# Kernel tuning notes

Measured on AMD Instinct MI355X. Metric: run time of the kernel, lower is better.

## Reference

```python
import jax, jax.numpy as jnp
import numpy as np

N = 50000      # nodes
E = 800000     # edges (avg degree 16)
IN = 100       # in_channels (hard-coded LayerNorm(100))
H = 128        # hidden_channels
G = 512        # num graphs in batch
C = 2          # num_classes
EPS = 1e-5     # LayerNorm eps (torch default)


def setup_inputs() -> dict:
    key = jax.random.key(0)
    ks = jax.random.split(key, 12)
    x = jax.random.normal(ks[0], (N, IN), dtype=jnp.float32)
    edge_index = jax.random.randint(ks[1], (2, E), 0, N, dtype=jnp.int64)
    edge_weight = jax.random.uniform(ks[2], (E,), dtype=jnp.float32)
    batch = jnp.sort(jax.random.randint(ks[3], (N,), 0, G, dtype=jnp.int64))
    # LayerNorm params (identity init, as torch)
    ln_g0, ln_b0 = jnp.ones((IN,), jnp.float32), jnp.zeros((IN,), jnp.float32)
    ln_g1, ln_b1 = jnp.ones((H,), jnp.float32), jnp.zeros((H,), jnp.float32)
    ln_g2, ln_b2 = jnp.ones((H,), jnp.float32), jnp.zeros((H,), jnp.float32)
    # GCNConv weights (glorot-ish scale) and biases
    W0 = jax.random.normal(ks[4], (IN, H), jnp.float32) / np.float32(np.sqrt(IN))
    b0 = jnp.zeros((H,), jnp.float32)
    W1 = jax.random.normal(ks[5], (H, H), jnp.float32) / np.float32(np.sqrt(H))
    b1 = jnp.zeros((H,), jnp.float32)
    W2 = jax.random.normal(ks[6], (H, H), jnp.float32) / np.float32(np.sqrt(H))
    b2 = jnp.zeros((H,), jnp.float32)
    # Final classifier
    Wlin = jax.random.normal(ks[7], (H, C), jnp.float32) / np.float32(np.sqrt(H))
    blin = jnp.zeros((C,), jnp.float32)
    return {"x": x, "edge_index": edge_index, "edge_weight": edge_weight,
            "batch": batch,
            "ln_g0": ln_g0, "ln_b0": ln_b0, "ln_g1": ln_g1, "ln_b1": ln_b1,
            "ln_g2": ln_g2, "ln_b2": ln_b2,
            "W0": W0, "b0": b0, "W1": W1, "b1": b1, "W2": W2, "b2": b2,
            "Wlin": Wlin, "blin": blin}


def _layernorm(h, g, b):
    m = jnp.mean(h, axis=-1, keepdims=True)
    v = jnp.mean(jnp.square(h - m), axis=-1, keepdims=True)
    return (h - m) * jax.lax.rsqrt(v + EPS) * g + b


def _gcn_conv(h, W, b, src, dst, edge_weight):
    # GCNConv(normalize=False): linear transform, edge gather scaled by
    # edge_weight, scatter-add to destination nodes, plus bias.
    hW = h @ W                                  # [N, H]
    msg = hW[src] * edge_weight[:, None]        # [E, H]
    agg = jax.ops.segment_sum(msg, dst, num_segments=N)  # [N, H]
    return agg + b


def reference(x, edge_index, edge_weight, batch,
              ln_g0, ln_b0, ln_g1, ln_b1, ln_g2, ln_b2,
              W0, b0, W1, b1, W2, b2, Wlin, blin):
    src, dst = edge_index[0], edge_index[1]
    layers = [(ln_g0, ln_b0, W0, b0), (ln_g1, ln_b1, W1, b1), (ln_g2, ln_b2, W2, b2)]
    h = x
    for (g, bb, W, cb) in layers:
        h = _layernorm(h, g, bb)
        h = _gcn_conv(h, W, cb, src, dst, edge_weight)
        h = jax.nn.relu(h)  # dropout is identity in eval mode
    # global mean pool over graphs
    sums = jax.ops.segment_sum(h, batch, num_segments=G)                       # [G, H]
    cnt = jax.ops.segment_sum(jnp.ones((N, 1), h.dtype), batch, num_segments=G)
    pooled = sums / jnp.maximum(cnt, 1.0)
    return pooled @ Wlin + blin  # [G, C]
```

## Files before the change

kernel.cpp:

```cpp
#include <hip/hip_runtime.h>
#include <hip/hip_bf16.h>

#define NN 50000
#define NE 800000
#define NG 512
#define HD 128
#define EPS 1e-5f
#define L1B 196
#define EPB 4096
#define NL1 ((NE + EPB - 1) / EPB)

typedef __attribute__((ext_vector_type(8))) short short8;
typedef __attribute__((ext_vector_type(4))) float f32x4;

__device__ __forceinline__ float bfu(unsigned short u) {
    return __uint_as_float((unsigned)u << 16);
}

__global__ __launch_bounds__(256) void k_init(int* __restrict__ gtot,
                                              float* __restrict__ pooled,
                                              const float* __restrict__ W0,
                                              const float* __restrict__ W1,
                                              const float* __restrict__ W2,
                                              __hip_bfloat16* __restrict__ bp) {
    const int i = blockIdx.x * 256 + threadIdx.x;
    if (i < L1B) gtot[i] = 0;
    if (i < NG * HD) pooled[i] = 0.f;
    if (i < 3 * 2048) {
        const int layer = i >> 11;
        const int f     = i & 2047;
        const int tile  = f >> 8, kk = (f >> 6) & 3, lane = f & 63;
        const int col   = tile * 16 + (lane & 15);
        const int kbase = kk * 32 + ((lane >> 4) << 3);
        const float* W  = (layer == 0) ? W0 : (layer == 1) ? W1 : W2;
        const int Klim  = (layer == 0) ? 100 : 128;
        alignas(16) __hip_bfloat16 o[8];
#pragma unroll
        for (int j = 0; j < 8; ++j) {
            const int k = kbase + j;
            o[j] = __float2bfloat16((k < Klim) ? W[(size_t)k * HD + col] : 0.f);
        }
        *(float4*)&bp[(size_t)i * 8] = *(const float4*)o;
    }
}

__global__ __launch_bounds__(256) void k_histL1(const int* __restrict__ dstv,
                                                int* __restrict__ gtot, int E) {
    __shared__ int h[L1B];
    const int t  = threadIdx.x;
    const int e0 = blockIdx.x * EPB;
    const int e1 = (e0 + EPB < E) ? (e0 + EPB) : E;
    for (int i = t; i < L1B; i += 256) h[i] = 0;
    __syncthreads();
    for (int e = e0 + t; e < e1; e += 256) atomicAdd(&h[dstv[e] >> 8], 1);
    __syncthreads();
    for (int i = t; i < L1B; i += 256)
        if (h[i]) atomicAdd(&gtot[i], h[i]);
}

__global__ __launch_bounds__(256) void k_scan196(const int* __restrict__ gtot,
                                                 int* __restrict__ gbase,
                                                 int* __restrict__ gcursor,
                                                 int* __restrict__ row_ptr) {
    __shared__ int s[256];
    const int t = threadIdx.x;
    const int v = (t < L1B) ? gtot[t] : 0;
    s[t] = v;
    __syncthreads();
    for (int off = 1; off < 256; off <<= 1) {
        int u = (t >= off) ? s[t - off] : 0;
        __syncthreads();
        s[t] += u;
        __syncthreads();
    }
    const int ex = s[t] - v;
    if (t < L1B) { gbase[t] = ex; gcursor[t] = ex; }
    if (t == 0) { gbase[L1B] = NE; row_ptr[NN] = NE; }
}

__global__ __launch_bounds__(256) void k_binL1(const int* __restrict__ srcv,
                                               const int* __restrict__ dstv,
                                               const float* __restrict__ ewt,
                                               int* __restrict__ gcursor,
                                               int2* __restrict__ stage, int E) {
    __shared__ int hist[L1B], lstart[L1B], gbase[L1B], lcur[L1B];
    __shared__ int s[256];
    __shared__ int2 lsort[EPB];
    const int t  = threadIdx.x;
    const int e0 = blockIdx.x * EPB;
    const int e1 = (e0 + EPB < E) ? (e0 + EPB) : E;
    for (int i = t; i < L1B; i += 256) hist[i] = 0;
    __syncthreads();
    for (int e = e0 + t; e < e1; e += 256)
        atomicAdd(&hist[dstv[e] >> 8], 1);
    __syncthreads();
    {
        const int v = (t < L1B) ? hist[t] : 0;
        s[t] = v;
        __syncthreads();
        for (int off = 1; off < 256; off <<= 1) {
            int u = (t >= off) ? s[t - off] : 0;
            __syncthreads();
            s[t] += u;
            __syncthreads();
        }
        if (t < L1B) {
            const int ex = s[t] - v;
            lstart[t] = ex;
            lcur[t]   = ex;
            gbase[t]  = v ? atomicAdd(&gcursor[t], v) : 0;
        }
    }
    __syncthreads();
    for (int e = e0 + t; e < e1; e += 256) {
        const int d = dstv[e];
        const int r = atomicAdd(&lcur[d >> 8], 1);
        lsort[r] = make_int2((d << 16) | srcv[e], __float_as_int(ewt[e]));
    }
    __syncthreads();
    const int n = e1 - e0;
    for (int i = t; i < n; i += 256) {
        const int2 el = lsort[i];
        const unsigned b = ((unsigned)el.x) >> 24;
        stage[gbase[b] + (i - lstart[b])] = el;
    }
}

__global__ __launch_bounds__(256) void k_binL2(const int2* __restrict__ stage,
                                               const int* __restrict__ gbase,
                                               int* __restrict__ row_ptr,
                                               int2* __restrict__ cw) {
    __shared__ int cnt[256], s[256], cur[256];
    const int t    = threadIdx.x;
    const int b    = blockIdx.x;
    const int d0   = b << 8;
    const int nd   = (NN - d0 < 256) ? (NN - d0) : 256;
    const int base = gbase[b];
    const int end  = gbase[b + 1];
    cnt[t] = 0;
    __syncthreads();
    for (int i = base + t; i < end; i += 256) {
        const unsigned dst = ((unsigned)stage[i].x) >> 16;
        atomicAdd(&cnt[dst - d0], 1);
    }
    __syncthreads();
    {
        const int v = cnt[t];
        s[t] = v;
        __syncthreads();
        for (int off = 1; off < 256; off <<= 1) {
            int u = (t >= off) ? s[t - off] : 0;
            __syncthreads();
            s[t] += u;
            __syncthreads();
        }
        const int ex = base + s[t] - v;
        cur[t] = ex;
        if (t < nd) row_ptr[d0 + t] = ex;
    }
    __syncthreads();
    for (int i = base + t; i < end; i += 256) {
        const int2 el = stage[i];
        const unsigned dst = ((unsigned)el.x) >> 16;
        const int p = atomicAdd(&cur[dst - d0], 1);
        cw[p] = make_int2(el.x & 0xFFFF, el.y);
    }
}

__device__ __forceinline__ void mfma_gemm_store(const __hip_bfloat16 (*hb)[136],
                                                const __hip_bfloat16* __restrict__ bp,
                                                __hip_bfloat16* __restrict__ hwb,
                                                int t, int r0) {
    const int wave = t >> 6, lane = t & 63;
    const int rw   = wave * 16;
    const int arow = rw + (lane & 15);
    const int acol = ((lane >> 4) << 3);
    short8 a[4];
#pragma unroll
    for (int kk = 0; kk < 4; ++kk)
        a[kk] = *(const short8*)&hb[arow][kk * 32 + acol];

    f32x4 acc[8] = {};
    const short8* bfr = (const short8*)bp;
#pragma unroll
    for (int tile = 0; tile < 8; ++tile) {
#pragma unroll
        for (int kk = 0; kk < 4; ++kk) {
            const short8 bb = bfr[(tile * 4 + kk) * 64 + lane];
            acc[tile] = __builtin_amdgcn_mfma_f32_16x16x32_bf16(a[kk], bb, acc[tile], 0, 0, 0);
        }
    }
    const int baser = r0 + rw + ((lane >> 4) << 2);
    const int bcol  = lane & 15;
#pragma unroll
    for (int tile = 0; tile < 8; ++tile) {
        const int col = tile * 16 + bcol;
#pragma unroll
        for (int j = 0; j < 4; ++j) {
            const int row = baser + j;
            if (row < NN) hwb[(size_t)row * HD + col] = __float2bfloat16(acc[tile][j]);
        }
    }
}

__global__ __launch_bounds__(256, 3) void k_ln_gemm_f32(const float* __restrict__ hin,
                                                        const float* __restrict__ g,
                                                        const float* __restrict__ b,
                                                        const __hip_bfloat16* __restrict__ bp,
                                                        __hip_bfloat16* __restrict__ hwb) {
    constexpr int K  = 100;
    constexpr int SK = K + 4;
    __shared__ float hs[64][SK];
    __shared__ __hip_bfloat16 hb[64][136];
    const int t  = threadIdx.x;
    const int r0 = blockIdx.x * 64;
    {
        const float4* src4 = (const float4*)(hin + (size_t)r0 * K);
        const int valid_rows = (NN - r0 < 64) ? (NN - r0) : 64;
        const int maxf = valid_rows * K;
        for (int i = t; i < 64 * K / 4; i += 256) {
            int f = i * 4;
            float4 v = (f < maxf) ? src4[i] : make_float4(0.f, 0.f, 0.f, 0.f);
            int r = f / K, k = f - r * K;
            *(float4*)&hs[r][k] = v;
        }
    }
    __syncthreads();
    {
        const int row = t >> 2, l = t & 3;
        float s = 0.f, s2 = 0.f;
        for (int k = l; k < K; k += 4) { float v = hs[row][k]; s += v; s2 += v * v; }
        s  += __shfl_xor(s, 1);  s2 += __shfl_xor(s2, 1);
        s  += __shfl_xor(s, 2);  s2 += __shfl_xor(s2, 2);
        const float mean = s / (float)K;
        const float var  = s2 / (float)K - mean * mean;
        const float rstd = rsqrtf(var + EPS);
        for (int k = l; k < K; k += 4)
            hb[row][k] = __float2bfloat16((hs[row][k] - mean) * rstd * g[k] + b[k]);
        for (int k = K + l; k < 128; k += 4)
            hb[row][k] = __float2bfloat16(0.f);
    }
    __syncthreads();
    mfma_gemm_store(hb, bp, hwb, t, r0);
}

__global__ __launch_bounds__(256, 4) void k_ln_gemm_b16(const __hip_bfloat16* __restrict__ hin,
                                                        const float* __restrict__ g,
                                                        const float* __restrict__ b,
                                                        const __hip_bfloat16* __restrict__ bp,
                                                        __hip_bfloat16* __restrict__ hwb) {
    __shared__ __hip_bfloat16 hb[64][136];
    const int t  = threadIdx.x;
    const int r0 = blockIdx.x * 64;
    {
        const float4* src4 = (const float4*)(hin + (size_t)r0 * HD);
        const int valid_rows = (NN - r0 < 64) ? (NN - r0) : 64;
        const int maxv = valid_rows * 16;
        for (int i = t; i < 1024; i += 256) {
            float4 v = (i < maxv) ? src4[i] : make_float4(0.f, 0.f, 0.f, 0.f);
            const int r = i >> 4, k = (i & 15) * 8;
            *(float4*)&hb[r][k] = v;
        }
    }
    __syncthreads();
    {
        const int row = t >> 2, l = t & 3;
        float s = 0.f, s2 = 0.f;
        for (int k = l; k < 128; k += 4) {
            const float v = __bfloat162float(hb[row][k]);
            s += v; s2 += v * v;
        }
        s  += __shfl_xor(s, 1);  s2 += __shfl_xor(s2, 1);
        s  += __shfl_xor(s, 2);  s2 += __shfl_xor(s2, 2);
        const float mean = s / 128.f;
        const float var  = s2 / 128.f - mean * mean;
        const float rstd = rsqrtf(var + EPS);
        for (int k = l; k < 128; k += 4)
            hb[row][k] = __float2bfloat16((__bfloat162float(hb[row][k]) - mean) * rstd * g[k] + b[k]);
    }
    __syncthreads();
    mfma_gemm_store(hb, bp, hwb, t, r0);
}

__device__ __forceinline__ float4 agg_row(const __hip_bfloat16* __restrict__ hwb,
                                          const int2* __restrict__ cw,
                                          const float* __restrict__ bias,
                                          int e0, int e1, size_t coff) {
    float4 acc = {0.f, 0.f, 0.f, 0.f};
    int e = e0;
    for (; e + 8 <= e1; e += 8) {
        int2 c[8];
#pragma unroll
        for (int j = 0; j < 8; ++j) c[j] = cw[e + j];
        ushort4 r[8];
#pragma unroll
        for (int j = 0; j < 8; ++j)
            r[j] = *(const ushort4*)(hwb + (size_t)c[j].x * HD + coff);
#pragma unroll
        for (int j = 0; j < 8; ++j) {
            const float w = __int_as_float(c[j].y);
            acc.x += w * bfu(r[j].x);
            acc.y += w * bfu(r[j].y);
            acc.z += w * bfu(r[j].z);
            acc.w += w * bfu(r[j].w);
        }
    }
    if (e + 4 <= e1) {
        int2 c[4];
#pragma unroll
        for (int j = 0; j < 4; ++j) c[j] = cw[e + j];
        ushort4 r[4];
#pragma unroll
        for (int j = 0; j < 4; ++j)
            r[j] = *(const ushort4*)(hwb + (size_t)c[j].x * HD + coff);
#pragma unroll
        for (int j = 0; j < 4; ++j) {
            const float w = __int_as_float(c[j].y);
            acc.x += w * bfu(r[j].x);
            acc.y += w * bfu(r[j].y);
            acc.z += w * bfu(r[j].z);
            acc.w += w * bfu(r[j].w);
        }
        e += 4;
    }
    for (; e < e1; ++e) {
        const int2 c = cw[e];
        const float w = __int_as_float(c.y);
        const ushort4 rv = *(const ushort4*)(hwb + (size_t)c.x * HD + coff);
        acc.x += w * bfu(rv.x);
        acc.y += w * bfu(rv.y);
        acc.z += w * bfu(rv.z);
        acc.w += w * bfu(rv.w);
    }
    const float4 bb = *(const float4*)(bias + coff);
    float4 o;
    o.x = fmaxf(acc.x + bb.x, 0.f);
    o.y = fmaxf(acc.y + bb.y, 0.f);
    o.z = fmaxf(acc.z + bb.z, 0.f);
    o.w = fmaxf(acc.w + bb.w, 0.f);
    return o;
}

__global__ __launch_bounds__(256) void k_aggregate(const __hip_bfloat16* __restrict__ hwb,
                                                   const int* __restrict__ row_ptr,
                                                   const int2* __restrict__ cw,
                                                   const float* __restrict__ bias,
                                                   __hip_bfloat16* __restrict__ hout, int n) {
    const int t    = threadIdx.x;
    const int grp  = t >> 5;
    const int lane = t & 31;
    const int node = blockIdx.x * 8 + grp;
    if (node >= n) return;
    const size_t coff = (size_t)lane * 4;
    float4 o = agg_row(hwb, cw, bias, row_ptr[node], row_ptr[node + 1], coff);
    alignas(8) __hip_bfloat16 ob[4] = {
        __float2bfloat16(o.x), __float2bfloat16(o.y),
        __float2bfloat16(o.z), __float2bfloat16(o.w)};
    *(ushort4*)(hout + (size_t)node * HD + coff) = *(const ushort4*)ob;
}

__global__ __launch_bounds__(256) void k_aggpool(const __hip_bfloat16* __restrict__ hwb,
                                                 const int* __restrict__ row_ptr,
                                                 const int2* __restrict__ cw,
                                                 const float* __restrict__ bias,
                                                 const int* __restrict__ batch,
                                                 float* __restrict__ pooled, int n) {
    __shared__ float lds[8][128];
    __shared__ int gof[8];
    const int t    = threadIdx.x;
    const int grp  = t >> 5;
    const int lane = t & 31;
    const int node = blockIdx.x * 8 + grp;
    const size_t coff = (size_t)lane * 4;
    float4 o = {0.f, 0.f, 0.f, 0.f};
    if (node < n)
        o = agg_row(hwb, cw, bias, row_ptr[node], row_ptr[node + 1], coff);
    *(float4*)&lds[grp][lane * 4] = o;
    if (lane == 0) gof[grp] = (node < n) ? batch[node] : -1;
    __syncthreads();
    if (t < 128) {
        float sum = 0.f;
        int curg = gof[0];
#pragma unroll
        for (int r = 0; r < 8; ++r) {
            const int gr = gof[r];
            if (gr != curg) {
                if (curg >= 0) atomicAdd(&pooled[curg * HD + t], sum);
                sum = 0.f;
                curg = gr;
            }
            if (gr >= 0) sum += lds[r][t];
        }
        if (curg >= 0) atomicAdd(&pooled[curg * HD + t], sum);
    }
}

__global__ __launch_bounds__(128) void k_linout(const float* __restrict__ pooled,
                                                const int* __restrict__ batch,
                                                const float* __restrict__ Wlin,
                                                const float* __restrict__ blin,
                                                float* __restrict__ out, int n) {
    __shared__ float red[2][128];
    const int gph = blockIdx.x;
    const int c   = threadIdx.x;
    int lo = 0, hi = n;
    while (lo < hi) { int mid = (lo + hi) >> 1; if (batch[mid] < gph) lo = mid + 1; else hi = mid; }
    const int start = lo;
    hi = n;
    while (lo < hi) { int mid = (lo + hi) >> 1; if (batch[mid] < gph + 1) lo = mid + 1; else hi = mid; }
    const float cnt = (float)(lo - start);
    const float pv = pooled[gph * HD + c] / fmaxf(cnt, 1.0f);
    red[0][c] = pv * Wlin[c * 2 + 0];
    red[1][c] = pv * Wlin[c * 2 + 1];
    __syncthreads();
    for (int off = 64; off; off >>= 1) {
        if (c < off) { red[0][c] += red[0][c + off]; red[1][c] += red[1][c + off]; }
        __syncthreads();
    }
    if (c == 0) {
        out[gph * 2 + 0] = red[0][0] + blin[0];
        out[gph * 2 + 1] = red[1][0] + blin[1];
    }
}

extern "C" void kernel_launch(void* const* d_in, const int* in_sizes, int n_in,
                              void* d_out, int out_size, void* d_ws, size_t ws_size,
                              hipStream_t stream) {
    const float* x     = (const float*)d_in[0];
    const int*   ei    = (const int*)d_in[1];
    const float* ewt   = (const float*)d_in[2];
    const int*   batch = (const int*)d_in[3];
    const float* ln_g0 = (const float*)d_in[4];
    const float* ln_b0 = (const float*)d_in[5];
    const float* ln_g1 = (const float*)d_in[6];
    const float* ln_b1 = (const float*)d_in[7];
    const float* ln_g2 = (const float*)d_in[8];
    const float* ln_b2 = (const float*)d_in[9];
    const float* W0    = (const float*)d_in[10];
    const float* b0    = (const float*)d_in[11];
    const float* W1    = (const float*)d_in[12];
    const float* b1    = (const float*)d_in[13];
    const float* W2    = (const float*)d_in[14];
    const float* b2    = (const float*)d_in[15];
    const float* Wlin  = (const float*)d_in[16];
    const float* blin  = (const float*)d_in[17];
    float* out = (float*)d_out;

    const int* srcv = ei;
    const int* dstv = ei + NE;

    char* ws = (char*)d_ws;
    size_t o = 0;
    auto carve = [&](size_t bytes) { void* p = ws + o; o += (bytes + 255) & ~(size_t)255; return p; };
    int*   row_ptr = (int*)carve(sizeof(int) * (NN + 1));
    int*   gtot    = (int*)carve(sizeof(int) * L1B);
    int*   gbase   = (int*)carve(sizeof(int) * (L1B + 1));
    int*   gcursor = (int*)carve(sizeof(int) * L1B);
    float* pooled  = (float*)carve(sizeof(float) * NG * HD);
    int2*  cw      = (int2*)carve(sizeof(int2) * NE);
    int2*  stage   = (int2*)carve(sizeof(int2) * NE);
    __hip_bfloat16* bpack = (__hip_bfloat16*)carve(sizeof(__hip_bfloat16) * 3 * 2048 * 8);
    __hip_bfloat16* hwb   = (__hip_bfloat16*)carve(sizeof(__hip_bfloat16) * NN * HD);
    __hip_bfloat16* hA    = (__hip_bfloat16*)carve(sizeof(__hip_bfloat16) * NN * HD);
    __hip_bfloat16* hB    = (__hip_bfloat16*)carve(sizeof(__hip_bfloat16) * NN * HD);
    (void)ws_size; (void)n_in; (void)in_sizes; (void)out_size;

    k_init<<<257, 256, 0, stream>>>(gtot, pooled, W0, W1, W2, bpack);

    k_histL1<<<NL1, 256, 0, stream>>>(dstv, gtot, NE);
    k_scan196<<<1, 256, 0, stream>>>(gtot, gbase, gcursor, row_ptr);
    k_binL1<<<NL1, 256, 0, stream>>>(srcv, dstv, ewt, gcursor, stage, NE);
    k_binL2<<<L1B, 256, 0, stream>>>(stage, gbase, row_ptr, cw);

    const int GEMM_GRID = (NN + 63) / 64;
    const int AGG_GRID  = (NN + 7) / 8;

    k_ln_gemm_f32<<<GEMM_GRID, 256, 0, stream>>>(x, ln_g0, ln_b0, bpack, hwb);
    k_aggregate<<<AGG_GRID, 256, 0, stream>>>(hwb, row_ptr, cw, b0, hA, NN);
    k_ln_gemm_b16<<<GEMM_GRID, 256, 0, stream>>>(hA, ln_g1, ln_b1, bpack + 2048 * 8, hwb);
    k_aggregate<<<AGG_GRID, 256, 0, stream>>>(hwb, row_ptr, cw, b1, hB, NN);
    k_ln_gemm_b16<<<GEMM_GRID, 256, 0, stream>>>(hB, ln_g2, ln_b2, bpack + 2 * 2048 * 8, hwb);
    k_aggpool<<<AGG_GRID, 256, 0, stream>>>(hwb, row_ptr, cw, b2, batch, pooled, NN);
    k_linout<<<NG, 128, 0, stream>>>(pooled, batch, Wlin, blin, out, NN);
}
```

Baseline: 207.7 us.

## Balance edge work across 8-node blocks with LDS atomic accumulation

Each aggregation block now splits the combined edge range of its 8 destination nodes evenly across its 8 groups, instead of giving one node per group. Groups accumulate per-destination partial sums and flush them into an LDS accumulator with shared-memory atomics when the destination changes. The low byte of each destination index is packed into the upper bits of the CSR source field so the row can be recovered. The aim is to remove load imbalance from varying node degree, at the cost of LDS atomics, extra bit ops and a dependence on NN being a multiple of 8.

```diff
diff --git a/kernel.cpp b/kernel.cpp
--- a/kernel.cpp
+++ b/kernel.cpp
@@ -163,7 +163,7 @@
         const int2 el = stage[i];
         const unsigned dst = ((unsigned)el.x) >> 16;
         const int p = atomicAdd(&cur[dst - d0], 1);
-        cw[p] = make_int2(el.x & 0xFFFF, el.y);
+        cw[p] = make_int2((el.x & 0xFFFF) | (int)((dst & 255u) << 16), el.y);
     }
 }
 
@@ -282,63 +282,73 @@
     mfma_gemm_store(hb, bp, hwb, t, r0);
 }
 
-__device__ __forceinline__ float4 agg_row(const __hip_bfloat16* __restrict__ hwb,
+__device__ __forceinline__ void agg_block(const __hip_bfloat16* __restrict__ hwb,
                                           const int2* __restrict__ cw,
-                                          const float* __restrict__ bias,
-                                          int e0, int e1, size_t coff) {
-    float4 acc = {0.f, 0.f, 0.f, 0.f};
-    int e = e0;
-    for (; e + 8 <= e1; e += 8) {
+                                          float (*acc)[128],
+                                          int n0, int e0, int e1,
+                                          int grp, int lane) {
+    const size_t coff = (size_t)lane * 4;
+    const int len = e1 - e0;
+    const int es  = e0 + ((len * grp) >> 3);
+    const int ee  = e0 + ((len * (grp + 1)) >> 3);
+    const int nbase = n0 & 255;
+    float4 a = {0.f, 0.f, 0.f, 0.f};
+    int rcur = -1;
+    int e = es;
+    for (; e + 8 <= ee; e += 8) {
         int2 c[8];
 #pragma unroll
         for (int j = 0; j < 8; ++j) c[j] = cw[e + j];
         ushort4 r[8];
 #pragma unroll
         for (int j = 0; j < 8; ++j)
-            r[j] = *(const ushort4*)(hwb + (size_t)c[j].x * HD + coff);
+            r[j] = *(const ushort4*)(hwb + (size_t)(c[j].x & 0xFFFF) * HD + coff);
 #pragma unroll
         for (int j = 0; j < 8; ++j) {
+            const int rr = (c[j].x >> 16) - nbase;
+            if (rr != rcur) {
+                if (rcur >= 0) {
+                    atomicAdd(&acc[rcur][lane * 4 + 0], a.x);
+                    atomicAdd(&acc[rcur][lane * 4 + 1], a.y);
+                    atomicAdd(&acc[rcur][lane * 4 + 2], a.z);
+                    atomicAdd(&acc[rcur][lane * 4 + 3], a.w);
+                }
+                a = make_float4(0.f, 0.f, 0.f, 0.f);
+                rcur = rr;
+            }
             const float w = __int_as_float(c[j].y);
-            acc.x += w * bfu(r[j].x);
-            acc.y += w * bfu(r[j].y);
-            acc.z += w * bfu(r[j].z);
-            acc.w += w * bfu(r[j].w);
-        }
-    }
-    if (e + 4 <= e1) {
-        int2 c[4];
-#pragma unroll
-        for (int j = 0; j < 4; ++j) c[j] = cw[e + j];
-        ushort4 r[4];
-#pragma unroll
-        for (int j = 0; j < 4; ++j)
-            r[j] = *(const ushort4*)(hwb + (size_t)c[j].x * HD + coff);
-#pragma unroll
-        for (int j = 0; j < 4; ++j) {
-            const float w = __int_as_float(c[j].y);
-            acc.x += w * bfu(r[j].x);
-            acc.y += w * bfu(r[j].y);
-            acc.z += w * bfu(r[j].z);
-            acc.w += w * bfu(r[j].w);
-        }
-        e += 4;
-    }
-    for (; e < e1; ++e) {
+            a.x += w * bfu(r[j].x);
+            a.y += w * bfu(r[j].y);
+            a.z += w * bfu(r[j].z);
+            a.w += w * bfu(r[j].w);
+        }
+    }
+    for (; e < ee; ++e) {
         const int2 c = cw[e];
+        const ushort4 rv = *(const ushort4*)(hwb + (size_t)(c.x & 0xFFFF) * HD + coff);
+        const int rr = (c.x >> 16) - nbase;
+        if (rr != rcur) {
+            if (rcur >= 0) {
+                atomicAdd(&acc[rcur][lane * 4 + 0], a.x);
+                atomicAdd(&acc[rcur][lane * 4 + 1], a.y);
+                atomicAdd(&acc[rcur][lane * 4 + 2], a.z);
+                atomicAdd(&acc[rcur][lane * 4 + 3], a.w);
+            }
+            a = make_float4(0.f, 0.f, 0.f, 0.f);
+            rcur = rr;
+        }
         const float w = __int_as_float(c.y);
-        const ushort4 rv = *(const ushort4*)(hwb + (size_t)c.x * HD + coff);
-        acc.x += w * bfu(rv.x);
-        acc.y += w * bfu(rv.y);
-        acc.z += w * bfu(rv.z);
-        acc.w += w * bfu(rv.w);
-    }
-    const float4 bb = *(const float4*)(bias + coff);
-    float4 o;
-    o.x = fmaxf(acc.x + bb.x, 0.f);
-    o.y = fmaxf(acc.y + bb.y, 0.f);
-    o.z = fmaxf(acc.z + bb.z, 0.f);
-    o.w = fmaxf(acc.w + bb.w, 0.f);
-    return o;
+        a.x += w * bfu(rv.x);
+        a.y += w * bfu(rv.y);
+        a.z += w * bfu(rv.z);
+        a.w += w * bfu(rv.w);
+    }
+    if (rcur >= 0) {
+        atomicAdd(&acc[rcur][lane * 4 + 0], a.x);
+        atomicAdd(&acc[rcur][lane * 4 + 1], a.y);
+        atomicAdd(&acc[rcur][lane * 4 + 2], a.z);
+        atomicAdd(&acc[rcur][lane * 4 + 3], a.w);
+    }
 }
 
 __global__ __launch_bounds__(256) void k_aggregate(const __hip_bfloat16* __restrict__ hwb,
@@ -346,17 +356,27 @@
                                                    const int2* __restrict__ cw,
                                                    const float* __restrict__ bias,
                                                    __hip_bfloat16* __restrict__ hout, int n) {
+    __shared__ float acc[8][128];
     const int t    = threadIdx.x;
     const int grp  = t >> 5;
     const int lane = t & 31;
-    const int node = blockIdx.x * 8 + grp;
-    if (node >= n) return;
-    const size_t coff = (size_t)lane * 4;
-    float4 o = agg_row(hwb, cw, bias, row_ptr[node], row_ptr[node + 1], coff);
+    const int n0   = blockIdx.x * 8;
+    for (int i = t; i < 1024; i += 256) ((float*)acc)[i] = 0.f;
+    const int e0 = row_ptr[n0];
+    const int e1 = row_ptr[n0 + 8];
+    __syncthreads();
+    agg_block(hwb, cw, acc, n0, e0, e1, grp, lane);
+    __syncthreads();
+    const int row = t >> 5;
+    const int ch  = (t & 31) * 4;
+    const float4 bb = *(const float4*)(bias + ch);
+    const float4 av = *(const float4*)&acc[row][ch];
     alignas(8) __hip_bfloat16 ob[4] = {
-        __float2bfloat16(o.x), __float2bfloat16(o.y),
-        __float2bfloat16(o.z), __float2bfloat16(o.w)};
-    *(ushort4*)(hout + (size_t)node * HD + coff) = *(const ushort4*)ob;
+        __float2bfloat16(fmaxf(av.x + bb.x, 0.f)),
+        __float2bfloat16(fmaxf(av.y + bb.y, 0.f)),
+        __float2bfloat16(fmaxf(av.z + bb.z, 0.f)),
+        __float2bfloat16(fmaxf(av.w + bb.w, 0.f))};
+    *(ushort4*)(hout + (size_t)(n0 + row) * HD + ch) = *(const ushort4*)ob;
 }
 
 __global__ __launch_bounds__(256) void k_aggpool(const __hip_bfloat16* __restrict__ hwb,
@@ -365,18 +385,30 @@
                                                  const float* __restrict__ bias,
                                                  const int* __restrict__ batch,
                                                  float* __restrict__ pooled, int n) {
-    __shared__ float lds[8][128];
+    __shared__ float acc[8][128];
     __shared__ int gof[8];
     const int t    = threadIdx.x;
     const int grp  = t >> 5;
     const int lane = t & 31;
-    const int node = blockIdx.x * 8 + grp;
-    const size_t coff = (size_t)lane * 4;
-    float4 o = {0.f, 0.f, 0.f, 0.f};
-    if (node < n)
-        o = agg_row(hwb, cw, bias, row_ptr[node], row_ptr[node + 1], coff);
-    *(float4*)&lds[grp][lane * 4] = o;
-    if (lane == 0) gof[grp] = (node < n) ? batch[node] : -1;
+    const int n0   = blockIdx.x * 8;
+    for (int i = t; i < 1024; i += 256) ((float*)acc)[i] = 0.f;
+    if (t < 8) gof[t] = batch[n0 + t];
+    const int e0 = row_ptr[n0];
+    const int e1 = row_ptr[n0 + 8];
+    __syncthreads();
+    agg_block(hwb, cw, acc, n0, e0, e1, grp, lane);
+    __syncthreads();
+    {
+        const int row = t >> 5;
+        const int ch  = (t & 31) * 4;
+        const float4 bb = *(const float4*)(bias + ch);
+        float4 av = *(const float4*)&acc[row][ch];
+        av.x = fmaxf(av.x + bb.x, 0.f);
+        av.y = fmaxf(av.y + bb.y, 0.f);
+        av.z = fmaxf(av.z + bb.z, 0.f);
+        av.w = fmaxf(av.w + bb.w, 0.f);
+        *(float4*)&acc[row][ch] = av;
+    }
     __syncthreads();
     if (t < 128) {
         float sum = 0.f;
@@ -385,13 +417,13 @@
         for (int r = 0; r < 8; ++r) {
             const int gr = gof[r];
             if (gr != curg) {
-                if (curg >= 0) atomicAdd(&pooled[curg * HD + t], sum);
+                atomicAdd(&pooled[curg * HD + t], sum);
                 sum = 0.f;
                 curg = gr;
             }
-            if (gr >= 0) sum += lds[r][t];
-        }
-        if (curg >= 0) atomicAdd(&pooled[curg * HD + t], sum);
+            sum += acc[r][t];
+        }
+        atomicAdd(&pooled[curg * HD + t], sum);
     }
 }
 
@@ -473,7 +505,7 @@
     k_binL2<<<L1B, 256, 0, stream>>>(stage, gbase, row_ptr, cw);
 
     const int GEMM_GRID = (NN + 63) / 64;
-    const int AGG_GRID  = (NN + 7) / 8;
+    const int AGG_GRID  = NN / 8;
 
     k_ln_gemm_f32<<<GEMM_GRID, 256, 0, stream>>>(x, ln_g0, ln_b0, bpack, hwb);
     k_aggregate<<<AGG_GRID, 256, 0, stream>>>(hwb, row_ptr, cw, b0, hA, NN);
```

New measurement: 321.3 us. 54.7% more time.

## Fuse edge aggregation with next layer's LayerNorm and GEMM

Applied to the files above, without the earlier changes.

Replaces the separate aggregate kernel and LN+GEMM kernel with one kernel per layer. Each block aggregates 64 node rows (8 per 32-lane group), computes LayerNorm via warp shuffles, writes bf16 rows into LDS, then runs the MFMA GEMM. This removes the round trip of the intermediate activation through global memory and one launch per layer. The cost is that each block now gathers 64 rows serially per group, which may lower parallelism and latency hiding in the gather phase. Ping-pong buffers replace the three activation buffers.

```diff
diff --git a/kernel.cpp b/kernel.cpp
--- a/kernel.cpp
+++ b/kernel.cpp
@@ -244,44 +244,6 @@
     mfma_gemm_store(hb, bp, hwb, t, r0);
 }
 
-__global__ __launch_bounds__(256, 4) void k_ln_gemm_b16(const __hip_bfloat16* __restrict__ hin,
-                                                        const float* __restrict__ g,
-                                                        const float* __restrict__ b,
-                                                        const __hip_bfloat16* __restrict__ bp,
-                                                        __hip_bfloat16* __restrict__ hwb) {
-    __shared__ __hip_bfloat16 hb[64][136];
-    const int t  = threadIdx.x;
-    const int r0 = blockIdx.x * 64;
-    {
-        const float4* src4 = (const float4*)(hin + (size_t)r0 * HD);
-        const int valid_rows = (NN - r0 < 64) ? (NN - r0) : 64;
-        const int maxv = valid_rows * 16;
-        for (int i = t; i < 1024; i += 256) {
-            float4 v = (i < maxv) ? src4[i] : make_float4(0.f, 0.f, 0.f, 0.f);
-            const int r = i >> 4, k = (i & 15) * 8;
-            *(float4*)&hb[r][k] = v;
-        }
-    }
-    __syncthreads();
-    {
-        const int row = t >> 2, l = t & 3;
-        float s = 0.f, s2 = 0.f;
-        for (int k = l; k < 128; k += 4) {
-            const float v = __bfloat162float(hb[row][k]);
-            s += v; s2 += v * v;
-        }
-        s  += __shfl_xor(s, 1);  s2 += __shfl_xor(s2, 1);
-        s  += __shfl_xor(s, 2);  s2 += __shfl_xor(s2, 2);
-        const float mean = s / 128.f;
-        const float var  = s2 / 128.f - mean * mean;
-        const float rstd = rsqrtf(var + EPS);
-        for (int k = l; k < 128; k += 4)
-            hb[row][k] = __float2bfloat16((__bfloat162float(hb[row][k]) - mean) * rstd * g[k] + b[k]);
-    }
-    __syncthreads();
-    mfma_gemm_store(hb, bp, hwb, t, r0);
-}
-
 __device__ __forceinline__ float4 agg_row(const __hip_bfloat16* __restrict__ hwb,
                                           const int2* __restrict__ cw,
                                           const float* __restrict__ bias,
@@ -341,22 +303,48 @@
     return o;
 }
 
-__global__ __launch_bounds__(256) void k_aggregate(const __hip_bfloat16* __restrict__ hwb,
-                                                   const int* __restrict__ row_ptr,
-                                                   const int2* __restrict__ cw,
-                                                   const float* __restrict__ bias,
-                                                   __hip_bfloat16* __restrict__ hout, int n) {
+__global__ __launch_bounds__(256) void k_agg_ln_gemm(const __hip_bfloat16* __restrict__ hwb_in,
+                                                     const int* __restrict__ row_ptr,
+                                                     const int2* __restrict__ cw,
+                                                     const float* __restrict__ bias,
+                                                     const float* __restrict__ g,
+                                                     const float* __restrict__ b,
+                                                     const __hip_bfloat16* __restrict__ bp,
+                                                     __hip_bfloat16* __restrict__ hwb_out) {
+    __shared__ __hip_bfloat16 hb[64][136];
     const int t    = threadIdx.x;
     const int grp  = t >> 5;
     const int lane = t & 31;
-    const int node = blockIdx.x * 8 + grp;
-    if (node >= n) return;
+    const int r0   = blockIdx.x * 64;
     const size_t coff = (size_t)lane * 4;
-    float4 o = agg_row(hwb, cw, bias, row_ptr[node], row_ptr[node + 1], coff);
-    alignas(8) __hip_bfloat16 ob[4] = {
-        __float2bfloat16(o.x), __float2bfloat16(o.y),
-        __float2bfloat16(o.z), __float2bfloat16(o.w)};
-    *(ushort4*)(hout + (size_t)node * HD + coff) = *(const ushort4*)ob;
+    const float4 gg = *(const float4*)(g + coff);
+    const float4 gb = *(const float4*)(b + coff);
+#pragma unroll
+    for (int i = 0; i < 8; ++i) {
+        const int row  = grp * 8 + i;
+        const int node = r0 + row;
+        float4 o = {0.f, 0.f, 0.f, 0.f};
+        if (node < NN) {
+            o = agg_row(hwb_in, cw, bias, row_ptr[node], row_ptr[node + 1], coff);
+            float s  = o.x + o.y + o.z + o.w;
+            float s2 = o.x * o.x + o.y * o.y + o.z * o.z + o.w * o.w;
+#pragma unroll
+            for (int m = 1; m < 32; m <<= 1) { s += __shfl_xor(s, m); s2 += __shfl_xor(s2, m); }
+            const float mean = s * (1.f / 128.f);
+            const float var  = s2 * (1.f / 128.f) - mean * mean;
+            const float rstd = rsqrtf(var + EPS);
+            o.x = (o.x - mean) * rstd * gg.x + gb.x;
+            o.y = (o.y - mean) * rstd * gg.y + gb.y;
+            o.z = (o.z - mean) * rstd * gg.z + gb.z;
+            o.w = (o.w - mean) * rstd * gg.w + gb.w;
+        }
+        alignas(8) __hip_bfloat16 ob[4] = {
+            __float2bfloat16(o.x), __float2bfloat16(o.y),
+            __float2bfloat16(o.z), __float2bfloat16(o.w)};
+        *(ushort4*)&hb[row][lane * 4] = *(const ushort4*)ob;
+    }
+    __syncthreads();
+    mfma_gemm_store(hb, bp, hwb_out, t, r0);
 }
 
 __global__ __launch_bounds__(256) void k_aggpool(const __hip_bfloat16* __restrict__ hwb,
@@ -460,9 +448,8 @@
     int2*  cw      = (int2*)carve(sizeof(int2) * NE);
     int2*  stage   = (int2*)carve(sizeof(int2) * NE);
     __hip_bfloat16* bpack = (__hip_bfloat16*)carve(sizeof(__hip_bfloat16) * 3 * 2048 * 8);
-    __hip_bfloat16* hwb   = (__hip_bfloat16*)carve(sizeof(__hip_bfloat16) * NN * HD);
-    __hip_bfloat16* hA    = (__hip_bfloat16*)carve(sizeof(__hip_bfloat16) * NN * HD);
-    __hip_bfloat16* hB    = (__hip_bfloat16*)carve(sizeof(__hip_bfloat16) * NN * HD);
+    __hip_bfloat16* hwbA  = (__hip_bfloat16*)carve(sizeof(__hip_bfloat16) * NN * HD);
+    __hip_bfloat16* hwbB  = (__hip_bfloat16*)carve(sizeof(__hip_bfloat16) * NN * HD);
     (void)ws_size; (void)n_in; (void)in_sizes; (void)out_size;
 
     k_init<<<257, 256, 0, stream>>>(gtot, pooled, W0, W1, W2, bpack);
@@ -473,13 +460,13 @@
     k_binL2<<<L1B, 256, 0, stream>>>(stage, gbase, row_ptr, cw);
 
     const int GEMM_GRID = (NN + 63) / 64;
-    const int AGG_GRID  = (NN + 7) / 8;
-
-    k_ln_gemm_f32<<<GEMM_GRID, 256, 0, stream>>>(x, ln_g0, ln_b0, bpack, hwb);
-    k_aggregate<<<AGG_GRID, 256, 0, stream>>>(hwb, row_ptr, cw, b0, hA, NN);
-    k_ln_gemm_b16<<<GEMM_GRID, 256, 0, stream>>>(hA, ln_g1, ln_b1, bpack + 2048 * 8, hwb);
-    k_aggregate<<<AGG_GRID, 256, 0, stream>>>(hwb, row_ptr, cw, b1, hB, NN);
-    k_ln_gemm_b16<<<GEMM_GRID, 256, 0, stream>>>(hB, ln_g2, ln_b2, bpack + 2 * 2048 * 8, hwb);
-    k_aggpool<<<AGG_GRID, 256, 0, stream>>>(hwb, row_ptr, cw, b2, batch, pooled, NN);
+    const int AGG_GRID  = NN / 8;
+
+    k_ln_gemm_f32<<<GEMM_GRID, 256, 0, stream>>>(x, ln_g0, ln_b0, bpack, hwbA);
+    k_agg_ln_gemm<<<GEMM_GRID, 256, 0, stream>>>(hwbA, row_ptr, cw, b0,
+                                                 ln_g1, ln_b1, bpack + 2048 * 8, hwbB);
+    k_agg_ln_gemm<<<GEMM_GRID, 256, 0, stream>>>(hwbB, row_ptr, cw, b1,
+                                                 ln_g2, ln_b2, bpack + 2 * 2048 * 8, hwbA);
+    k_aggpool<<<AGG_GRID, 256, 0, stream>>>(hwbA, row_ptr, cw, b2, batch, pooled, NN);
     k_linout<<<NG, 128, 0, stream>>>(pooled, batch, Wlin, blin, out, NN);
 }
```

Measured after the change: 211.7 us. About the same (+1.9%).
